# Optimization experiments

Measured on AMD Instinct MI355X. Metric: run time of the kernel, lower is better.

The kernel has to match this reference:

```python
import jax, jax.numpy as jnp
import numpy as np

CHUNK_SIZE = 8       # init arg: samples averaged per center
IP_WEIGHT = 0.5      # init arg: lerp weight toward chunk center
WEIGHT = 1.0 / 8     # hardcoded per-sample loss weight in the module
GROUP = 4            # negative-mining exclusion window is hardcoded to groups of 4
N, D = 8192, 2048


def setup_inputs() -> dict:
    key = jax.random.key(0)
    x = jax.random.normal(key, (N, D), dtype=jnp.float32)
    return {"x": x}


def reference(x):
    n, d = x.shape
    # chunk centers: mean over each contiguous chunk of CHUNK_SIZE rows
    centers = x.reshape(n // CHUNK_SIZE, CHUNK_SIZE, d).mean(axis=1)        # [n/cs, d]
    center_per_row = jnp.repeat(centers, CHUNK_SIZE, axis=0)                # [n, d]
    # torch.lerp(x_i, center, w) = x_i + w*(center - x_i)
    x_pos = x + IP_WEIGHT * (center_per_row - x)                            # [n, d]

    # negative mining: most-similar row (largest dot product) whose index is
    # OUTSIDE the caller's group-of-4 window [i - i%4, i + 3 - i%4]
    sim = jnp.matmul(x, x.T)                                                # [n, n]
    grp = jnp.arange(n) // GROUP
    same_group = grp[:, None] == grp[None, :]
    neg_idx = jnp.argmax(jnp.where(same_group, -jnp.inf, sim), axis=1)      # [n]
    x_neg = x[neg_idx]                                                      # [n, d]

    # per-sample L1 (mean over features), contrastive ratio, weighted sum
    d_ap = jnp.mean(jnp.abs(x - x_pos), axis=1)                             # [n]
    d_an = jnp.mean(jnp.abs(x - x_neg), axis=1)                             # [n]
    return jnp.sum(WEIGHT * d_ap / (d_an + 1e-7))
```

## Files before the change

### kernel.cpp

```cpp
#include <hip/hip_runtime.h>
#include <hip/hip_bf16.h>
#include <float.h>
#include <math.h>

#define N 8192
#define D 2048
#define CS 8
#define NT 64

#define BM 128
#define BN 128
#define BK 128

typedef __attribute__((ext_vector_type(4))) int   i32x4;
typedef __attribute__((ext_vector_type(8))) int   i32x8;
typedef __attribute__((ext_vector_type(4))) float f32x4;
typedef __attribute__((ext_vector_type(2))) float f32x2;

__device__ __forceinline__ void g2l16(const void* g, void* l) {
    __builtin_amdgcn_global_load_lds(
        (const __attribute__((address_space(1))) void*)g,
        (__attribute__((address_space(3))) void*)l, 16, 0, 0);
}

__global__ __launch_bounds__(256) void chunk_kernel(
    const float* __restrict__ x, int* __restrict__ xq, float* __restrict__ d_ap) {
    const int c = blockIdx.x;
    const int tid = threadIdx.x;
    const float4* xr4 = (const float4*)(x + (size_t)c * CS * D);

    float dap[CS];
    #pragma unroll
    for (int r = 0; r < CS; ++r) dap[r] = 0.f;

    #pragma unroll
    for (int h = 0; h < 2; ++h) {
        const int col = h * 256 + tid;
        float4 v[CS];
        float4 cen = make_float4(0, 0, 0, 0);
        #pragma unroll
        for (int r = 0; r < CS; ++r) {
            v[r] = xr4[r * 512 + col];
            cen.x += v[r].x; cen.y += v[r].y; cen.z += v[r].z; cen.w += v[r].w;
        }
        cen.x *= 0.125f; cen.y *= 0.125f; cen.z *= 0.125f; cen.w *= 0.125f;
        #pragma unroll
        for (int r = 0; r < CS; ++r) {
            int p = __builtin_amdgcn_cvt_pk_fp8_f32(v[r].x, v[r].y, 0, false);
            p     = __builtin_amdgcn_cvt_pk_fp8_f32(v[r].z, v[r].w, p, true);
            xq[(size_t)(c * CS + r) * 512 + col] = p;
            dap[r] += fabsf(v[r].x - cen.x) + fabsf(v[r].y - cen.y)
                    + fabsf(v[r].z - cen.z) + fabsf(v[r].w - cen.w);
        }
    }
    #pragma unroll
    for (int r = 0; r < CS; ++r)
        #pragma unroll
        for (int m = 1; m <= 32; m <<= 1) dap[r] += __shfl_xor(dap[r], m, 64);

    __shared__ float sred[CS][4];
    const int lane = tid & 63, wave = tid >> 6;
    if (lane == 0)
        #pragma unroll
        for (int r = 0; r < CS; ++r) sred[r][wave] = dap[r];
    __syncthreads();
    if (tid < CS) {
        const float s = sred[tid][0] + sred[tid][1] + sred[tid][2] + sred[tid][3];
        d_ap[c * CS + tid] = 0.5f * s / (float)D;
    }
}

__global__ __launch_bounds__(256, 3) void gemm_argmax_kernel(
    const char* __restrict__ xq,
    float* __restrict__ pmax, int* __restrict__ pidx) {
    __shared__ __align__(16) char sA[BM * BK];
    __shared__ __align__(16) char sB[BN * BK];

    const int t = blockIdx.x;
    int bi = (int)((129.0 - sqrt((double)(129 * 129 - 8 * t))) * 0.5);
    if (bi > 63) bi = 63;
    if (bi < 0) bi = 0;
    while ((bi + 1) * (129 - (bi + 1)) / 2 <= t) ++bi;
    while (bi * (129 - bi) / 2 > t) --bi;
    const int bj = bi + (t - bi * (129 - bi) / 2);
    const bool diag = (bi == bj);

    const int tid  = threadIdx.x;
    const int lane = tid & 63;
    const int wave = tid >> 6;
    const int quad = lane >> 4;
    const int l15  = lane & 15;

    const int i0 = bi * BM;
    const int j0 = bj * BN;
    const int wr = (wave >> 1) * 64;
    const int wc = (wave & 1) * 64;

    int aoff[4], boff[4];
    #pragma unroll
    for (int tt = 0; tt < 4; ++tt) {
        const int arow = wr + tt * 16 + l15;
        aoff[tt] = arow * 128 + (((2 * quad) ^ (arow & 7)) << 4);
        const int brow = wc + tt * 16 + l15;
        boff[tt] = brow * 128 + (((2 * quad) ^ (brow & 7)) << 4);
    }
    const char* gsrcA[4]; const char* gsrcB[4];
    char* ldstA[4]; char* ldstB[4];
    #pragma unroll
    for (int c = 0; c < 4; ++c) {
        const int segbase = wave * 64 + c * 256;
        const int s   = segbase + lane;
        const int row = s >> 3;
        const int pc  = s & 7;
        const int gk  = (pc ^ (row & 7)) << 4;
        gsrcA[c] = xq + (size_t)(i0 + row) * D + gk;
        gsrcB[c] = xq + (size_t)(j0 + row) * D + gk;
        ldstA[c] = sA + segbase * 16;
        ldstB[c] = sB + segbase * 16;
    }

    f32x4 acc[4][4] = {};

    for (int kk = 0; kk < D; kk += BK) {
        #pragma unroll
        for (int c = 0; c < 4; ++c) { g2l16(gsrcA[c], ldstA[c]); g2l16(gsrcB[c], ldstB[c]); }
        #pragma unroll
        for (int c = 0; c < 4; ++c) { gsrcA[c] += BK; gsrcB[c] += BK; }
        __syncthreads();

        i32x8 af[4], bfr[4];
        #pragma unroll
        for (int tt = 0; tt < 4; ++tt) {
            const i32x4 alo = *(const i32x4*)(sA + aoff[tt]);
            const i32x4 ahi = *(const i32x4*)(sA + (aoff[tt] ^ 16));
            const i32x4 blo = *(const i32x4*)(sB + boff[tt]);
            const i32x4 bhi = *(const i32x4*)(sB + (boff[tt] ^ 16));
            #pragma unroll
            for (int e = 0; e < 4; ++e) {
                af[tt][e] = alo[e];  af[tt][e + 4] = ahi[e];
                bfr[tt][e] = blo[e]; bfr[tt][e + 4] = bhi[e];
            }
        }
        #pragma unroll
        for (int ti = 0; ti < 4; ++ti)
            #pragma unroll
            for (int tj = 0; tj < 4; ++tj)
                acc[ti][tj] = __builtin_amdgcn_mfma_scale_f32_16x16x128_f8f6f4(
                    af[ti], bfr[tj], acc[ti][tj],
                    0, 0,
                    0, 0x7F7F7F7F,
                    0, 0x7F7F7F7F);
        __syncthreads();
    }

    float* rmax = (float*)(sA + 0);
    int*   ridx = (int*)  (sA + 1024);
    float* cmax = (float*)(sA + 2048);
    int*   cidx = (int*)  (sA + 3072);

    #pragma unroll
    for (int ti = 0; ti < 4; ++ti) {
        #pragma unroll
        for (int r = 0; r < 4; ++r) {
            const int li = wr + ti * 16 + quad * 4 + r;
            const int gi = i0 + li;
            float bv = -FLT_MAX; int bj_ = 0x7fffffff;
            #pragma unroll
            for (int tj = 0; tj < 4; ++tj) {
                const int gj = j0 + wc + tj * 16 + l15;
                const float vv = acc[ti][tj][r];
                const bool ok = !diag || ((gi >> 2) != (gj >> 2));
                if (ok && (vv > bv || (vv == bv && gj < bj_))) { bv = vv; bj_ = gj; }
            }
            #pragma unroll
            for (int m = 1; m <= 8; m <<= 1) {
                const float ov = __shfl_xor(bv, m, 64);
                const int   oj = __shfl_xor(bj_, m, 64);
                if (ov > bv || (ov == bv && oj < bj_)) { bv = ov; bj_ = oj; }
            }
            if (l15 == 0) { rmax[li * 2 + (wave & 1)] = bv; ridx[li * 2 + (wave & 1)] = bj_; }
        }
    }

    if (!diag) {
        #pragma unroll
        for (int tj = 0; tj < 4; ++tj) {
            float bv = -FLT_MAX; int bi_ = 0x7fffffff;
            #pragma unroll
            for (int ti = 0; ti < 4; ++ti)
                #pragma unroll
                for (int r = 0; r < 4; ++r) {
                    const int gi = i0 + wr + ti * 16 + quad * 4 + r;
                    const float vv = acc[ti][tj][r];
                    if (vv > bv || (vv == bv && gi < bi_)) { bv = vv; bi_ = gi; }
                }
            #pragma unroll
            for (int m = 16; m <= 32; m <<= 1) {
                const float ov = __shfl_xor(bv, m, 64);
                const int   oi = __shfl_xor(bi_, m, 64);
                if (ov > bv || (ov == bv && oi < bi_)) { bv = ov; bi_ = oi; }
            }
            if (quad == 0) {
                const int cj = wc + tj * 16 + l15;
                cmax[cj * 2 + (wave >> 1)] = bv; cidx[cj * 2 + (wave >> 1)] = bi_;
            }
        }
    }
    __syncthreads();

    if (tid < BM) {
        const float v0 = rmax[tid * 2], v1 = rmax[tid * 2 + 1];
        const int   a0 = ridx[tid * 2], a1 = ridx[tid * 2 + 1];
        float bv; int ba;
        if (v1 > v0 || (v1 == v0 && a1 < a0)) { bv = v1; ba = a1; }
        else                                  { bv = v0; ba = a0; }
        pmax[(size_t)(i0 + tid) * NT + bj] = bv;
        pidx[(size_t)(i0 + tid) * NT + bj] = ba;
    } else if (!diag) {
        const int c = tid - BM;
        const float v0 = cmax[c * 2], v1 = cmax[c * 2 + 1];
        const int   a0 = cidx[c * 2], a1 = cidx[c * 2 + 1];
        float bv; int ba;
        if (v1 > v0 || (v1 == v0 && a1 < a0)) { bv = v1; ba = a1; }
        else                                  { bv = v0; ba = a0; }
        pmax[(size_t)(j0 + c) * NT + bi] = bv;
        pidx[(size_t)(j0 + c) * NT + bi] = ba;
    }
}

__global__ __launch_bounds__(256) void neg_kernel(
    const int* __restrict__ xq, const float* __restrict__ d_ap,
    const float* __restrict__ pmax, const int* __restrict__ pidx,
    float* __restrict__ term) {
    const int i = blockIdx.x;
    const int tid = threadIdx.x;
    __shared__ int s_neg;
    __shared__ float red[4];

    if (tid < 64) {
        float bv = pmax[(size_t)i * NT + tid];
        int   bj = pidx[(size_t)i * NT + tid];
        #pragma unroll
        for (int m = 1; m <= 32; m <<= 1) {
            const float ov = __shfl_xor(bv, m, 64);
            const int   oj = __shfl_xor(bj, m, 64);
            if (ov > bv || (ov == bv && oj < bj)) { bv = ov; bj = oj; }
        }
        if (tid == 0) s_neg = bj;
    }
    __syncthreads();
    const int neg = s_neg;

    const int* xi = xq + (size_t)i * 512;
    const int* xn = xq + (size_t)neg * 512;
    float san = 0.f;
    #pragma unroll
    for (int c = tid; c < 512; c += 256) {
        const int a = xi[c], b = xn[c];
        const f32x2 alo = __builtin_amdgcn_cvt_pk_f32_fp8(a, false);
        const f32x2 ahi = __builtin_amdgcn_cvt_pk_f32_fp8(a, true);
        const f32x2 blo = __builtin_amdgcn_cvt_pk_f32_fp8(b, false);
        const f32x2 bhi = __builtin_amdgcn_cvt_pk_f32_fp8(b, true);
        san += fabsf(alo[0] - blo[0]) + fabsf(alo[1] - blo[1])
             + fabsf(ahi[0] - bhi[0]) + fabsf(ahi[1] - bhi[1]);
    }
    #pragma unroll
    for (int m = 1; m <= 32; m <<= 1) san += __shfl_xor(san, m, 64);
    const int lane = tid & 63, wave = tid >> 6;
    if (lane == 0) red[wave] = san;
    __syncthreads();
    if (tid == 0) {
        const float d_an = (red[0] + red[1] + red[2] + red[3]) / (float)D;
        term[i] = 0.125f * d_ap[i] / (d_an + 1e-7f);
    }
}

__global__ __launch_bounds__(256) void sum_kernel(
    const float* __restrict__ term, float* __restrict__ out) {
    const int tid = threadIdx.x;
    float s = 0.f;
    for (int i = tid; i < N; i += 256) s += term[i];
    #pragma unroll
    for (int m = 1; m <= 32; m <<= 1) s += __shfl_xor(s, m, 64);
    __shared__ float red[4];
    const int lane = tid & 63, wave = tid >> 6;
    if (lane == 0) red[wave] = s;
    __syncthreads();
    if (tid == 0) out[0] = red[0] + red[1] + red[2] + red[3];
}

extern "C" void kernel_launch(void* const* d_in, const int* in_sizes, int n_in,
                              void* d_out, int out_size, void* d_ws, size_t ws_size,
                              hipStream_t stream) {
    const float* x = (const float*)d_in[0];
    float* out = (float*)d_out;
    char* ws = (char*)d_ws;

    char* xq    = ws;
    float* pmax = (float*)(ws + (size_t)N * D);
    int*   pidx = (int*)((char*)pmax + (size_t)N * NT * 4);
    float* dap  = (float*)((char*)pidx + (size_t)N * NT * 4);
    float* term = dap + N;

    chunk_kernel<<<N / CS, 256, 0, stream>>>(x, (int*)xq, dap);
    gemm_argmax_kernel<<<NT * (NT + 1) / 2, 256, 0, stream>>>(xq, pmax, pidx);
    neg_kernel<<<N, 256, 0, stream>>>((const int*)xq, dap, pmax, pidx, term);
    sum_kernel<<<1, 256, 0, stream>>>(term, out);
}
```

Baseline: 226.0 us.

## Double-buffer LDS tiles so global loads overlap MFMA compute

Splits the shared-memory A/B tiles into two buffers and prefetches the next K-slice into one buffer while MFMAs consume the other. This hides global-to-LDS load latency behind compute and drops one barrier per iteration. LDS use per block doubles, so the launch-bounds occupancy hint drops from 3 to 2 blocks per CU, which reduces latency hiding through occupancy.

```diff
diff --git a/kernel.cpp b/kernel.cpp
--- a/kernel.cpp
+++ b/kernel.cpp
@@ -11,6 +11,7 @@
 #define BM 128
 #define BN 128
 #define BK 128
+#define KITERS (D / BK)
 
 typedef __attribute__((ext_vector_type(4))) int   i32x4;
 typedef __attribute__((ext_vector_type(8))) int   i32x8;
@@ -70,11 +71,11 @@
     }
 }
 
-__global__ __launch_bounds__(256, 3) void gemm_argmax_kernel(
+__global__ __launch_bounds__(256, 2) void gemm_argmax_kernel(
     const char* __restrict__ xq,
     float* __restrict__ pmax, int* __restrict__ pidx) {
-    __shared__ __align__(16) char sA[BM * BK];
-    __shared__ __align__(16) char sB[BN * BK];
+    __shared__ __align__(16) char sA0[BM * BK], sA1[BM * BK];
+    __shared__ __align__(16) char sB0[BN * BK], sB1[BN * BK];
 
     const int t = blockIdx.x;
     int bi = (int)((129.0 - sqrt((double)(129 * 129 - 8 * t))) * 0.5);
@@ -105,7 +106,7 @@
         boff[tt] = brow * 128 + (((2 * quad) ^ (brow & 7)) << 4);
     }
     const char* gsrcA[4]; const char* gsrcB[4];
-    char* ldstA[4]; char* ldstB[4];
+    int segoff[4];
     #pragma unroll
     for (int c = 0; c < 4; ++c) {
         const int segbase = wave * 64 + c * 256;
@@ -115,26 +116,28 @@
         const int gk  = (pc ^ (row & 7)) << 4;
         gsrcA[c] = xq + (size_t)(i0 + row) * D + gk;
         gsrcB[c] = xq + (size_t)(j0 + row) * D + gk;
-        ldstA[c] = sA + segbase * 16;
-        ldstB[c] = sB + segbase * 16;
+        segoff[c] = segbase * 16;
     }
 
     f32x4 acc[4][4] = {};
 
-    for (int kk = 0; kk < D; kk += BK) {
-        #pragma unroll
-        for (int c = 0; c < 4; ++c) { g2l16(gsrcA[c], ldstA[c]); g2l16(gsrcB[c], ldstB[c]); }
+    auto stage = [&](char* dA, char* dB) {
+        #pragma unroll
+        for (int c = 0; c < 4; ++c) {
+            g2l16(gsrcA[c], dA + segoff[c]);
+            g2l16(gsrcB[c], dB + segoff[c]);
+        }
         #pragma unroll
         for (int c = 0; c < 4; ++c) { gsrcA[c] += BK; gsrcB[c] += BK; }
-        __syncthreads();
-
+    };
+    auto compute = [&](const char* bufA, const char* bufB) {
         i32x8 af[4], bfr[4];
         #pragma unroll
         for (int tt = 0; tt < 4; ++tt) {
-            const i32x4 alo = *(const i32x4*)(sA + aoff[tt]);
-            const i32x4 ahi = *(const i32x4*)(sA + (aoff[tt] ^ 16));
-            const i32x4 blo = *(const i32x4*)(sB + boff[tt]);
-            const i32x4 bhi = *(const i32x4*)(sB + (boff[tt] ^ 16));
+            const i32x4 alo = *(const i32x4*)(bufA + aoff[tt]);
+            const i32x4 ahi = *(const i32x4*)(bufA + (aoff[tt] ^ 16));
+            const i32x4 blo = *(const i32x4*)(bufB + boff[tt]);
+            const i32x4 bhi = *(const i32x4*)(bufB + (boff[tt] ^ 16));
             #pragma unroll
             for (int e = 0; e < 4; ++e) {
                 af[tt][e] = alo[e];  af[tt][e + 4] = ahi[e];
@@ -150,13 +153,25 @@
                     0, 0,
                     0, 0x7F7F7F7F,
                     0, 0x7F7F7F7F);
+    };
+
+    stage(sA0, sB0);
+    __syncthreads();
+
+    #pragma unroll 1
+    for (int it = 0; it < KITERS; it += 2) {
+        stage(sA1, sB1);
+        compute(sA0, sB0);
         __syncthreads();
-    }
-
-    float* rmax = (float*)(sA + 0);
-    int*   ridx = (int*)  (sA + 1024);
-    float* cmax = (float*)(sA + 2048);
-    int*   cidx = (int*)  (sA + 3072);
+        if (it + 2 < KITERS) stage(sA0, sB0);
+        compute(sA1, sB1);
+        __syncthreads();
+    }
+
+    float* rmax = (float*)(sA0 + 0);
+    int*   ridx = (int*)  (sA0 + 1024);
+    float* cmax = (float*)(sA0 + 2048);
+    int*   cidx = (int*)  (sA0 + 3072);
 
     #pragma unroll
     for (int ti = 0; ti < 4; ++ti) {
```

Measured after the change: 254.4 us. 1.13x slower.

## Widen GEMM-argmax tile to 128x256 with 512-thread blocks over triangle supertiles

Applied to the files above, without the earlier changes.

Widens the symmetric FP8 GEMM tile from 128x128 to 128x256 and runs 8 waves per block. Work is enumerated over 1056 triangle supertiles, each covering two adjacent column tiles, with a separate diagonal mask for each half. The goal is better A-tile reuse and more MFMA work per LDS load and barrier, with fewer blocks. The trade-offs are more LDS per block (48KB), lower occupancy, and some redundant compute on supertiles that straddle the diagonal.

```diff
diff --git a/kernel.cpp b/kernel.cpp
--- a/kernel.cpp
+++ b/kernel.cpp
@@ -9,8 +9,10 @@
 #define NT 64
 
 #define BM 128
-#define BN 128
+#define BN 256
 #define BK 128
+#define KITERS (D / BK)
+#define NSUPER 1056
 
 typedef __attribute__((ext_vector_type(4))) int   i32x4;
 typedef __attribute__((ext_vector_type(8))) int   i32x8;
@@ -70,31 +72,31 @@
     }
 }
 
-__global__ __launch_bounds__(256, 3) void gemm_argmax_kernel(
+__global__ __launch_bounds__(512, 4) void gemm_argmax_kernel(
     const char* __restrict__ xq,
     float* __restrict__ pmax, int* __restrict__ pidx) {
     __shared__ __align__(16) char sA[BM * BK];
     __shared__ __align__(16) char sB[BN * BK];
 
     const int t = blockIdx.x;
-    int bi = (int)((129.0 - sqrt((double)(129 * 129 - 8 * t))) * 0.5);
-    if (bi > 63) bi = 63;
-    if (bi < 0) bi = 0;
-    while ((bi + 1) * (129 - (bi + 1)) / 2 <= t) ++bi;
-    while (bi * (129 - bi) / 2 > t) --bi;
-    const int bj = bi + (t - bi * (129 - bi) / 2);
-    const bool diag = (bi == bj);
+    int bi = 0, start = 0;
+    while (start + (32 - (bi >> 1)) <= t) { start += 32 - (bi >> 1); ++bi; }
+    const int J   = (bi >> 1) + (t - start);
+    const int bj0 = 2 * J;
+    const int i0  = bi * BM;
+    const int j0  = J * BN;
+    const bool diagL = (bj0 == bi);
+    const bool diagR = (bj0 + 1 == bi);
 
     const int tid  = threadIdx.x;
     const int lane = tid & 63;
     const int wave = tid >> 6;
     const int quad = lane >> 4;
     const int l15  = lane & 15;
-
-    const int i0 = bi * BM;
-    const int j0 = bj * BN;
-    const int wr = (wave >> 1) * 64;
-    const int wc = (wave & 1) * 64;
+    const int wm   = wave >> 2;
+    const int wn   = wave & 3;
+    const int wr   = wm * 64;
+    const int wc   = wn * 64;
 
     int aoff[4], boff[4];
     #pragma unroll
@@ -104,28 +106,37 @@
         const int brow = wc + tt * 16 + l15;
         boff[tt] = brow * 128 + (((2 * quad) ^ (brow & 7)) << 4);
     }
-    const char* gsrcA[4]; const char* gsrcB[4];
-    char* ldstA[4]; char* ldstB[4];
-    #pragma unroll
-    for (int c = 0; c < 4; ++c) {
-        const int segbase = wave * 64 + c * 256;
-        const int s   = segbase + lane;
-        const int row = s >> 3;
-        const int pc  = s & 7;
-        const int gk  = (pc ^ (row & 7)) << 4;
-        gsrcA[c] = xq + (size_t)(i0 + row) * D + gk;
-        gsrcB[c] = xq + (size_t)(j0 + row) * D + gk;
-        ldstA[c] = sA + segbase * 16;
-        ldstB[c] = sB + segbase * 16;
+    const char* gsrcA[2]; const char* gsrcB[4];
+    int soA[2], soB[4];
+    {
+        const int rsub = lane >> 3;
+        const int pc   = lane & 7;
+        const int gk   = (pc ^ rsub) << 4;
+        #pragma unroll
+        for (int c = 0; c < 2; ++c) {
+            const int g = wave + 8 * c;
+            gsrcA[c] = xq + (size_t)(i0 + g * 8 + rsub) * D + gk;
+            soA[c]   = g * 1024;
+        }
+        #pragma unroll
+        for (int c = 0; c < 4; ++c) {
+            const int g = wave + 8 * c;
+            gsrcB[c] = xq + (size_t)(j0 + g * 8 + rsub) * D + gk;
+            soB[c]   = g * 1024;
+        }
     }
 
     f32x4 acc[4][4] = {};
 
     for (int kk = 0; kk < D; kk += BK) {
         #pragma unroll
-        for (int c = 0; c < 4; ++c) { g2l16(gsrcA[c], ldstA[c]); g2l16(gsrcB[c], ldstB[c]); }
-        #pragma unroll
-        for (int c = 0; c < 4; ++c) { gsrcA[c] += BK; gsrcB[c] += BK; }
+        for (int c = 0; c < 2; ++c) g2l16(gsrcA[c], sA + soA[c]);
+        #pragma unroll
+        for (int c = 0; c < 4; ++c) g2l16(gsrcB[c], sB + soB[c]);
+        #pragma unroll
+        for (int c = 0; c < 2; ++c) gsrcA[c] += BK;
+        #pragma unroll
+        for (int c = 0; c < 4; ++c) gsrcB[c] += BK;
         __syncthreads();
 
         i32x8 af[4], bfr[4];
@@ -154,9 +165,12 @@
     }
 
     float* rmax = (float*)(sA + 0);
-    int*   ridx = (int*)  (sA + 1024);
-    float* cmax = (float*)(sA + 2048);
-    int*   cidx = (int*)  (sA + 3072);
+    int*   ridx = (int*)  (sA + 2048);
+    float* cmax = (float*)(sA + 4096);
+    int*   cidx = (int*)  (sA + 6144);
+
+    const int ct = wn >> 1;
+    const bool diagct = ct ? diagR : diagL;
 
     #pragma unroll
     for (int ti = 0; ti < 4; ++ti) {
@@ -169,7 +183,7 @@
             for (int tj = 0; tj < 4; ++tj) {
                 const int gj = j0 + wc + tj * 16 + l15;
                 const float vv = acc[ti][tj][r];
-                const bool ok = !diag || ((gi >> 2) != (gj >> 2));
+                const bool ok = !diagct || ((gi >> 2) != (gj >> 2));
                 if (ok && (vv > bv || (vv == bv && gj < bj_))) { bv = vv; bj_ = gj; }
             }
             #pragma unroll
@@ -178,11 +192,14 @@
                 const int   oj = __shfl_xor(bj_, m, 64);
                 if (ov > bv || (ov == bv && oj < bj_)) { bv = ov; bj_ = oj; }
             }
-            if (l15 == 0) { rmax[li * 2 + (wave & 1)] = bv; ridx[li * 2 + (wave & 1)] = bj_; }
-        }
-    }
-
-    if (!diag) {
+            if (l15 == 0) {
+                rmax[li * 4 + ct * 2 + (wn & 1)] = bv;
+                ridx[li * 4 + ct * 2 + (wn & 1)] = bj_;
+            }
+        }
+    }
+
+    if (!diagct) {
         #pragma unroll
         for (int tj = 0; tj < 4; ++tj) {
             float bv = -FLT_MAX; int bi_ = 0x7fffffff;
@@ -202,29 +219,35 @@
             }
             if (quad == 0) {
                 const int cj = wc + tj * 16 + l15;
-                cmax[cj * 2 + (wave >> 1)] = bv; cidx[cj * 2 + (wave >> 1)] = bi_;
-            }
-        }
-    }
-    __syncthreads();
-
-    if (tid < BM) {
-        const float v0 = rmax[tid * 2], v1 = rmax[tid * 2 + 1];
-        const int   a0 = ridx[tid * 2], a1 = ridx[tid * 2 + 1];
+                cmax[cj * 2 + wm] = bv; cidx[cj * 2 + wm] = bi_;
+            }
+        }
+    }
+    __syncthreads();
+
+    if (tid < 256) {
+        const int r  = tid & 127;
+        const int c2 = tid >> 7;
+        const float v0 = rmax[r * 4 + c2 * 2], v1 = rmax[r * 4 + c2 * 2 + 1];
+        const int   a0 = ridx[r * 4 + c2 * 2], a1 = ridx[r * 4 + c2 * 2 + 1];
         float bv; int ba;
         if (v1 > v0 || (v1 == v0 && a1 < a0)) { bv = v1; ba = a1; }
         else                                  { bv = v0; ba = a0; }
-        pmax[(size_t)(i0 + tid) * NT + bj] = bv;
-        pidx[(size_t)(i0 + tid) * NT + bj] = ba;
-    } else if (!diag) {
-        const int c = tid - BM;
-        const float v0 = cmax[c * 2], v1 = cmax[c * 2 + 1];
-        const int   a0 = cidx[c * 2], a1 = cidx[c * 2 + 1];
-        float bv; int ba;
-        if (v1 > v0 || (v1 == v0 && a1 < a0)) { bv = v1; ba = a1; }
-        else                                  { bv = v0; ba = a0; }
-        pmax[(size_t)(j0 + c) * NT + bi] = bv;
-        pidx[(size_t)(j0 + c) * NT + bi] = ba;
+        pmax[(size_t)(i0 + r) * NT + bj0 + c2] = bv;
+        pidx[(size_t)(i0 + r) * NT + bj0 + c2] = ba;
+    } else {
+        const int c = tid - 256;
+        const int ctc = c >> 7;
+        const bool skip = ctc ? diagR : diagL;
+        if (!skip) {
+            const float v0 = cmax[c * 2], v1 = cmax[c * 2 + 1];
+            const int   a0 = cidx[c * 2], a1 = cidx[c * 2 + 1];
+            float bv; int ba;
+            if (v1 > v0 || (v1 == v0 && a1 < a0)) { bv = v1; ba = a1; }
+            else                                  { bv = v0; ba = a0; }
+            pmax[(size_t)(j0 + c) * NT + bi] = bv;
+            pidx[(size_t)(j0 + c) * NT + bi] = ba;
+        }
     }
 }
 
@@ -303,7 +326,7 @@
     float* term = dap + N;
 
     chunk_kernel<<<N / CS, 256, 0, stream>>>(x, (int*)xq, dap);
-    gemm_argmax_kernel<<<NT * (NT + 1) / 2, 256, 0, stream>>>(xq, pmax, pidx);
+    gemm_argmax_kernel<<<NSUPER, 512, 0, stream>>>(xq, pmax, pidx);
     neg_kernel<<<N, 256, 0, stream>>>((const int*)xq, dap, pmax, pidx, term);
     sum_kernel<<<1, 256, 0, stream>>>(term, out);
 }
```

After: 267.8 us. +18.5%, slower.
